# Optimization experiments

Measured on AMD Instinct MI355X. Metric: run time of the kernel, lower is better.

## Reference

```python
import jax, jax.numpy as jnp
import numpy as np

B, N, C_IN, C_OUT, K, D_EMB = 64, 2048, 64, 64, 3, 10

def setup_inputs() -> dict:
    key = jax.random.key(0)
    k1, k2, k3, k4 = jax.random.split(key, 4)
    x = jax.random.normal(k1, (B, N, C_IN), dtype=jnp.float32)
    node_embeddings = jax.random.normal(k2, (N, D_EMB), dtype=jnp.float32)
    weights_pool = jax.random.normal(k3, (D_EMB, K, C_IN, C_OUT), dtype=jnp.float32) * 0.1
    bias_pool = jax.random.normal(k4, (D_EMB, C_OUT), dtype=jnp.float32) * 0.1
    return {"x": x, "node_embeddings": node_embeddings,
            "weights_pool": weights_pool, "bias_pool": bias_pool, "cheb_k": K}

def reference(x, node_embeddings, weights_pool, bias_pool, cheb_k):
    n = node_embeddings.shape[0]
    # adaptive adjacency: softmax over rows of relu(E E^T)
    supports = jax.nn.softmax(jax.nn.relu(node_embeddings @ node_embeddings.T), axis=1)  # [N,N]
    support_set = [jnp.eye(n, dtype=x.dtype), supports]
    for _ in range(2, cheb_k):
        support_set.append(2.0 * supports @ support_set[-1] - support_set[-2])
    supports_k = jnp.stack(support_set, axis=0)                     # [K,N,N]
    # per-node weights/bias generated from embedding
    weights = jnp.einsum('nd,dkio->nkio', node_embeddings, weights_pool)  # [N,K,Ci,Co]
    bias = node_embeddings @ bias_pool                               # [N,Co]
    # graph conv: gather Chebyshev-filtered features then per-node grouped GEMM
    x_g = jnp.einsum('knm,bmc->bnkc', supports_k, x)                 # [B,N,K,Ci]
    out = jnp.einsum('bnki,nkio->bno', x_g, weights) + bias          # [B,N,Co]
    return out
```

## Files before the change

### kernel.cpp

```cpp
#include <hip/hip_runtime.h>

typedef __attribute__((ext_vector_type(8))) short short8;
typedef __attribute__((ext_vector_type(4))) float f32x4;
typedef __attribute__((ext_vector_type(4))) unsigned short us4;
typedef __attribute__((ext_vector_type(8))) unsigned short us8;

constexpr int Bb = 64, Nn = 2048, CI = 64, CO = 64, KK = 3, DE = 10;
constexpr int NW = Bb * CI;
constexpr int WPSZ = KK * CI * CO;

__device__ __forceinline__ unsigned short f2bf(float f) {
  unsigned u = __float_as_uint(f);
  u += 0x7fff + ((u >> 16) & 1);
  return (unsigned short)(u >> 16);
}
__device__ __forceinline__ float bf2f(unsigned short h) {
  return __uint_as_float(((unsigned)h) << 16);
}
__device__ __forceinline__ void gl2lds16(const void* g, void* l) {
  __builtin_amdgcn_global_load_lds(
      (const __attribute__((address_space(1))) void*)g,
      (__attribute__((address_space(3))) void*)l, 16, 0, 0);
}

__global__ __launch_bounds__(256) void supports_kernel(
    const float* __restrict__ E, unsigned short* __restrict__ S) {
  const int n = blockIdx.x, t = threadIdx.x;
  __shared__ float red[256];
  float emb[DE];
#pragma unroll
  for (int d = 0; d < DE; d++) emb[d] = E[n * DE + d];
  float v[8], lmax = -1e30f;
#pragma unroll
  for (int j = 0; j < 8; j++) {
    const int m = t + j * 256;
    float dot = 0.f;
#pragma unroll
    for (int d = 0; d < DE; d++) dot += emb[d] * E[m * DE + d];
    v[j] = fmaxf(dot, 0.f);
    lmax = fmaxf(lmax, v[j]);
  }
  red[t] = lmax;
  __syncthreads();
  for (int s = 128; s > 0; s >>= 1) {
    if (t < s) red[t] = fmaxf(red[t], red[t + s]);
    __syncthreads();
  }
  const float rowmax = red[0];
  __syncthreads();
  float lsum = 0.f;
#pragma unroll
  for (int j = 0; j < 8; j++) { v[j] = __expf(v[j] - rowmax); lsum += v[j]; }
  red[t] = lsum;
  __syncthreads();
  for (int s = 128; s > 0; s >>= 1) {
    if (t < s) red[t] += red[t + s];
    __syncthreads();
  }
  const float inv = 1.f / red[0];
#pragma unroll
  for (int j = 0; j < 8; j++) S[(size_t)n * Nn + t + j * 256] = f2bf(v[j] * inv);
}

__global__ __launch_bounds__(256) void x2xt_kernel(
    const float* __restrict__ x, unsigned short* __restrict__ Xrow,
    unsigned short* __restrict__ XT) {
  __shared__ float T[64 * 65];
  const int b = blockIdx.x, n0 = blockIdx.y * 64, t = threadIdx.x;
  const int i4 = (t & 15) * 4;
#pragma unroll
  for (int j = 0; j < 4; j++) {
    const int r = j * 16 + (t >> 4);
    const float4 v =
        *(const float4*)(x + (size_t)b * (Nn * CI) + (size_t)(n0 + r) * CI + i4);
    us4 o; o.x = f2bf(v.x); o.y = f2bf(v.y); o.z = f2bf(v.z); o.w = f2bf(v.w);
    *(us4*)(Xrow + (size_t)(n0 + r) * NW + b * CI + i4) = o;
    T[r * 65 + i4 + 0] = v.x; T[r * 65 + i4 + 1] = v.y;
    T[r * 65 + i4 + 2] = v.z; T[r * 65 + i4 + 3] = v.w;
  }
  __syncthreads();
  const int i = t >> 2, c0 = (t & 3) * 16;
  us8 p0, p1;
#pragma unroll
  for (int j = 0; j < 8; j++) p0[j] = f2bf(T[(c0 + j) * 65 + i]);
#pragma unroll
  for (int j = 0; j < 8; j++) p1[j] = f2bf(T[(c0 + 8 + j) * 65 + i]);
  unsigned short* dst = XT + (size_t)(b * CI + i) * Nn + n0 + c0;
  *(us8*)(dst) = p0;
  *(us8*)(dst + 8) = p1;
}

__global__ __launch_bounds__(256) void mfma_gemm(
    const unsigned short* __restrict__ A, const unsigned short* __restrict__ Bt,
    const unsigned short* __restrict__ Xsub, unsigned short* __restrict__ Crow,
    unsigned short* __restrict__ Ct, int mode) {
  __shared__ unsigned short sm[16384];
  unsigned short* As = sm;
  unsigned short* Bs = sm + 8192;
  const int t = threadIdx.x, lane = t & 63, wave = t >> 6;
  const int n0 = blockIdx.x * 128, m0 = blockIdx.y * 128;
  const int wm = (wave & 1) * 64, wn = (wave >> 1) * 64;
  const int lr = lane & 15, lq = lane >> 4;

  f32x4 acc[4][4] = {};
  const int srow = lane >> 3;
  const int schunk = (lane & 7) ^ srow;

  for (int k0 = 0; k0 < 2048; k0 += 64) {
    __syncthreads();
#pragma unroll
    for (int j = 0; j < 4; j++) {
      const int r0 = (wave * 4 + j) * 8;
      gl2lds16(A  + (size_t)(m0 + r0 + srow) * 2048 + k0 + schunk * 8, As + r0 * 64);
      gl2lds16(Bt + (size_t)(n0 + r0 + srow) * 2048 + k0 + schunk * 8, Bs + r0 * 64);
    }
    __syncthreads();
#pragma unroll
    for (int ks = 0; ks < 2; ks++) {
      short8 af[4], bfr[4];
#pragma unroll
      for (int i = 0; i < 4; i++) {
        const int m = wm + i * 16 + lr;
        const int slot = (ks * 4 + lq) ^ (m & 7);
        af[i] = *(const short8*)(As + m * 64 + slot * 8);
      }
#pragma unroll
      for (int j = 0; j < 4; j++) {
        const int n = wn + j * 16 + lr;
        const int slot = (ks * 4 + lq) ^ (n & 7);
        bfr[j] = *(const short8*)(Bs + n * 64 + slot * 8);
      }
#pragma unroll
      for (int i = 0; i < 4; i++)
#pragma unroll
        for (int j = 0; j < 4; j++)
          acc[i][j] = __builtin_amdgcn_mfma_f32_16x16x32_bf16(af[i], bfr[j], acc[i][j], 0, 0, 0);
    }
  }

  __syncthreads();
#pragma unroll
  for (int i = 0; i < 4; i++) {
#pragma unroll
    for (int r = 0; r < 4; r++) {
      const int m = wm + i * 16 + lq * 4 + r;
      const int sw = (m & 7) ^ ((m >> 3) & 7);
#pragma unroll
      for (int j = 0; j < 4; j++) {
        const int n = wn + j * 16 + lr;
        sm[m * 128 + (((n >> 3) ^ sw) * 8) + (n & 7)] = f2bf(acc[i][j][r]);
      }
    }
  }
  __syncthreads();

  {
    const int rr = t >> 4, cc = (t & 15) * 8;
#pragma unroll
    for (int p = 0; p < 8; p++) {
      const int m = p * 16 + rr;
      const int slot = (cc >> 3) ^ (m & 7) ^ ((m >> 3) & 7);
      us8 v = *(const us8*)(sm + m * 128 + slot * 8);
      if (mode == 1) {
        const us8 xv = *(const us8*)(Xsub + (size_t)(m0 + m) * NW + n0 + cc);
#pragma unroll
        for (int q = 0; q < 8; q++) v[q] = f2bf(2.f * bf2f(v[q]) - bf2f(xv[q]));
      }
      *(us8*)(Crow + (size_t)(m0 + m) * NW + n0 + cc) = v;
    }
  }
  if (mode == 0) {
    const int w = t >> 4, mc = (t & 15) * 8;
#pragma unroll
    for (int p = 0; p < 8; p++) {
      const int n = p * 16 + w;
      us8 v;
#pragma unroll
      for (int q = 0; q < 8; q++) {
        const int m = mc + q;
        v[q] = sm[m * 128 + (((n >> 3) ^ (m & 7) ^ ((m >> 3) & 7)) * 8) + (n & 7)];
      }
      *(us8*)(Ct + (size_t)(n0 + n) * 2048 + m0 + mc) = v;
    }
  }
}

__global__ __launch_bounds__(256) void out_kernel(
    const unsigned short* __restrict__ Xrow, const unsigned short* __restrict__ XG1,
    const unsigned short* __restrict__ XG2, const float* __restrict__ E,
    const float* __restrict__ Wp, const float* __restrict__ bp,
    float* __restrict__ out) {
  constexpr int WP = 72;
  __shared__ unsigned short Wt[KK * CO * WP];
  __shared__ unsigned short Al[KK * Bb * CI];
  __shared__ float biasl[CO];

  const int n = blockIdx.x, t = threadIdx.x, lane = t & 63, wave = t >> 6;

  const unsigned short* srcs[KK] = {Xrow + (size_t)n * NW, XG1 + (size_t)n * NW,
                                    XG2 + (size_t)n * NW};
  const int srow = lane >> 3;
  const int schunk = (lane & 7) ^ srow;
#pragma unroll
  for (int j = 0; j < 6; j++) {
    const int r0 = (wave * 6 + j) * 8;
    const int c = r0 >> 6, b0 = r0 & 63;
    gl2lds16(srcs[c] + (b0 + srow) * 64 + schunk * 8, Al + r0 * 64);
  }

  float emb[DE];
#pragma unroll
  for (int d = 0; d < DE; d++) emb[d] = E[n * DE + d];

#pragma unroll
  for (int j = 0; j < 12; j++) {
    const int idx4 = j * 1024 + t * 4;
    const int c = j >> 2;
    const int i = (j * 16 + (t >> 4)) & 63;
    const int o = (t & 15) * 4;
    f32x4 w = {0.f, 0.f, 0.f, 0.f};
#pragma unroll
    for (int d = 0; d < DE; d++) {
      const float4 wp = *(const float4*)(Wp + (size_t)d * WPSZ + idx4);
      w[0] += emb[d] * wp.x; w[1] += emb[d] * wp.y;
      w[2] += emb[d] * wp.z; w[3] += emb[d] * wp.w;
    }
#pragma unroll
    for (int q = 0; q < 4; q++)
      Wt[c * (CO * WP) + (o + q) * WP + i] = f2bf(w[q]);
  }
  if (t < CO) {
    float bsum = 0.f;
#pragma unroll
    for (int d = 0; d < DE; d++) bsum += emb[d] * bp[d * CO + t];
    biasl[t] = bsum;
  }
  __syncthreads();

  const int lr = lane & 15, lq = lane >> 4;
  f32x4 acc[4] = {};
#pragma unroll
  for (int kt = 0; kt < 6; kt++) {
    const int c = kt >> 1;
    const int i0 = (kt & 1) * 32;
    const short8 bfrag = *(const short8*)(Wt + c * (CO * WP) +
                                          (wave * 16 + lr) * WP + i0 + lq * 8);
#pragma unroll
    for (int mt = 0; mt < 4; mt++) {
      const int b = mt * 16 + lr;
      const int chunk = (kt & 1) * 4 + lq;
      const int slot = chunk ^ (b & 7);
      const short8 afrag = *(const short8*)(Al + (c * 64 + b) * 64 + slot * 8);
      acc[mt] = __builtin_amdgcn_mfma_f32_16x16x32_bf16(afrag, bfrag, acc[mt], 0, 0, 0);
    }
  }

  const float bias_o = biasl[wave * 16 + lr];
#pragma unroll
  for (int mt = 0; mt < 4; mt++) {
#pragma unroll
    for (int r = 0; r < 4; r++) {
      const int b = mt * 16 + lq * 4 + r;
      out[(size_t)b * (Nn * CO) + (size_t)n * CO + wave * 16 + lr] =
          acc[mt][r] + bias_o;
    }
  }
}

extern "C" void kernel_launch(void* const* d_in, const int* in_sizes, int n_in,
                              void* d_out, int out_size, void* d_ws,
                              size_t ws_size, hipStream_t stream) {
  const float* x  = (const float*)d_in[0];
  const float* E  = (const float*)d_in[1];
  const float* Wp = (const float*)d_in[2];
  const float* bp = (const float*)d_in[3];
  float* out = (float*)d_out;

  unsigned short* S    = (unsigned short*)d_ws;
  unsigned short* XT   = S    + (size_t)Nn * Nn;
  unsigned short* Xrow = XT   + (size_t)NW * Nn;
  unsigned short* XG1T = Xrow + (size_t)Nn * NW;
  unsigned short* XG1r = XG1T + (size_t)NW * Nn;
  unsigned short* XG2r = XG1r + (size_t)Nn * NW;

  supports_kernel<<<Nn, 256, 0, stream>>>(E, S);
  x2xt_kernel<<<dim3(Bb, Nn / 64), 256, 0, stream>>>(x, Xrow, XT);

  dim3 g(NW / 128, Nn / 128);
  mfma_gemm<<<g, 256, 0, stream>>>(S, XT,   nullptr, XG1r, XG1T, 0);
  mfma_gemm<<<g, 256, 0, stream>>>(S, XG1T, Xrow,    XG2r, nullptr, 1);

  out_kernel<<<Nn, 256, 0, stream>>>(Xrow, XG1r, XG2r, E, Wp, bp, out);
}
```

Before: 236.2 us.

## Precompute per-node bf16 weights in separate kernel and stream them into out_kernel

Moves generation of the per-node weights and bias out of out_kernel into a new wgen_kernel. That kernel holds the weight-pool slices in registers and reuses them across 64 nodes, then writes bf16 weights in a swizzled layout that matches out_kernel's LDS pattern. out_kernel now loads those weights with async global-to-LDS copies, so each block no longer re-reads the full 10x12K float weight pool. The cost is an extra kernel launch and a write plus read of 2048x12K bf16 weights (about 50MB), which reuses the supports buffer in the reorganized workspace.

```diff
diff --git a/kernel.cpp b/kernel.cpp
--- a/kernel.cpp
+++ b/kernel.cpp
@@ -185,20 +185,79 @@
   }
 }
 
+__global__ __launch_bounds__(256) void wgen_kernel(
+    const float* __restrict__ E, const float* __restrict__ Wp,
+    const float* __restrict__ bp, unsigned short* __restrict__ W_all,
+    float* __restrict__ bias_all) {
+  constexpr int WSP = 24;
+  const int t = threadIdx.x, n0 = blockIdx.x * 64, c = blockIdx.y;
+  __shared__ float El[64 * DE];
+  __shared__ unsigned short Ws[4][64 * WSP];
+
+  for (int idx = t; idx < 64 * DE; idx += 256) El[idx] = E[n0 * DE + idx];
+  __syncthreads();
+
+  if (c == 0) {
+#pragma unroll
+    for (int j = 0; j < 16; j++) {
+      const int idx = j * 256 + t;
+      const int nl = idx >> 6, o = idx & 63;
+      float bsum = 0.f;
+#pragma unroll
+      for (int d = 0; d < DE; d++) bsum += El[nl * DE + d] * bp[d * CO + o];
+      bias_all[(size_t)(n0 + nl) * CO + o] = bsum;
+    }
+  }
+
+  const int o = t & 63, ig = t >> 6;
+  for (int p = 0; p < 4; p++) {
+    float wp[4][DE];
+#pragma unroll
+    for (int j = 0; j < 4; j++) {
+      const int i = p * 16 + ig * 4 + j;
+#pragma unroll
+      for (int d = 0; d < DE; d++)
+        wp[j][d] = Wp[(size_t)d * WPSZ + c * (CI * CO) + i * CO + o];
+    }
+    for (int g = 0; g < 16; g++) {
+#pragma unroll
+      for (int nl = 0; nl < 4; nl++) {
+        const int nn = g * 4 + nl;
+        us4 w;
+#pragma unroll
+        for (int j = 0; j < 4; j++) {
+          float acc = 0.f;
+#pragma unroll
+          for (int d = 0; d < DE; d++) acc += El[nn * DE + d] * wp[j][d];
+          w[j] = f2bf(acc);
+        }
+        *(us4*)&Ws[nl][o * WSP + ig * 4] = w;
+      }
+      __syncthreads();
+#pragma unroll
+      for (int rd = 0; rd < 2; rd++) {
+        const int idx = rd * 256 + t;
+        const int nl = idx >> 7, o2 = (idx >> 1) & 63, h = idx & 1;
+        const us8 v = *(const us8*)&Ws[nl][o2 * WSP + h * 8];
+        *(us8*)(W_all + (size_t)(n0 + g * 4 + nl) * WPSZ +
+                (c * 64 + o2) * 64 + p * 16 + h * 8) = v;
+      }
+      __syncthreads();
+    }
+  }
+}
+
 __global__ __launch_bounds__(256) void out_kernel(
     const unsigned short* __restrict__ Xrow, const unsigned short* __restrict__ XG1,
-    const unsigned short* __restrict__ XG2, const float* __restrict__ E,
-    const float* __restrict__ Wp, const float* __restrict__ bp,
-    float* __restrict__ out) {
-  constexpr int WP = 72;
-  __shared__ unsigned short Wt[KK * CO * WP];
+    const unsigned short* __restrict__ XG2, const unsigned short* __restrict__ W_all,
+    const float* __restrict__ bias_all, float* __restrict__ out) {
+  __shared__ unsigned short Wt[KK * CO * 64];
   __shared__ unsigned short Al[KK * Bb * CI];
-  __shared__ float biasl[CO];
 
   const int n = blockIdx.x, t = threadIdx.x, lane = t & 63, wave = t >> 6;
-
   const unsigned short* srcs[KK] = {Xrow + (size_t)n * NW, XG1 + (size_t)n * NW,
                                     XG2 + (size_t)n * NW};
+  const unsigned short* wsrc = W_all + (size_t)n * WPSZ;
   const int srow = lane >> 3;
   const int schunk = (lane & 7) ^ srow;
 #pragma unroll
@@ -206,56 +265,30 @@
     const int r0 = (wave * 6 + j) * 8;
     const int c = r0 >> 6, b0 = r0 & 63;
     gl2lds16(srcs[c] + (b0 + srow) * 64 + schunk * 8, Al + r0 * 64);
-  }
-
-  float emb[DE];
-#pragma unroll
-  for (int d = 0; d < DE; d++) emb[d] = E[n * DE + d];
-
-#pragma unroll
-  for (int j = 0; j < 12; j++) {
-    const int idx4 = j * 1024 + t * 4;
-    const int c = j >> 2;
-    const int i = (j * 16 + (t >> 4)) & 63;
-    const int o = (t & 15) * 4;
-    f32x4 w = {0.f, 0.f, 0.f, 0.f};
-#pragma unroll
-    for (int d = 0; d < DE; d++) {
-      const float4 wp = *(const float4*)(Wp + (size_t)d * WPSZ + idx4);
-      w[0] += emb[d] * wp.x; w[1] += emb[d] * wp.y;
-      w[2] += emb[d] * wp.z; w[3] += emb[d] * wp.w;
-    }
-#pragma unroll
-    for (int q = 0; q < 4; q++)
-      Wt[c * (CO * WP) + (o + q) * WP + i] = f2bf(w[q]);
-  }
-  if (t < CO) {
-    float bsum = 0.f;
-#pragma unroll
-    for (int d = 0; d < DE; d++) bsum += emb[d] * bp[d * CO + t];
-    biasl[t] = bsum;
-  }
-  __syncthreads();
+    gl2lds16(wsrc + (r0 + srow) * 64 + schunk * 8, Wt + r0 * 64);
+  }
 
   const int lr = lane & 15, lq = lane >> 4;
+  const float bias_o = bias_all[(size_t)n * CO + wave * 16 + lr];
+  __syncthreads();
+
   f32x4 acc[4] = {};
 #pragma unroll
   for (int kt = 0; kt < 6; kt++) {
     const int c = kt >> 1;
-    const int i0 = (kt & 1) * 32;
-    const short8 bfrag = *(const short8*)(Wt + c * (CO * WP) +
-                                          (wave * 16 + lr) * WP + i0 + lq * 8);
+    const int chunk = (kt & 1) * 4 + lq;
+    const int o = wave * 16 + lr;
+    const short8 bfrag =
+        *(const short8*)(Wt + (c * 64 + o) * 64 + (chunk ^ (o & 7)) * 8);
 #pragma unroll
     for (int mt = 0; mt < 4; mt++) {
       const int b = mt * 16 + lr;
-      const int chunk = (kt & 1) * 4 + lq;
-      const int slot = chunk ^ (b & 7);
-      const short8 afrag = *(const short8*)(Al + (c * 64 + b) * 64 + slot * 8);
+      const short8 afrag =
+          *(const short8*)(Al + (c * 64 + b) * 64 + (chunk ^ (b & 7)) * 8);
       acc[mt] = __builtin_amdgcn_mfma_f32_16x16x32_bf16(afrag, bfrag, acc[mt], 0, 0, 0);
     }
   }
 
-  const float bias_o = biasl[wave * 16 + lr];
 #pragma unroll
   for (int mt = 0; mt < 4; mt++) {
 #pragma unroll
@@ -276,12 +309,15 @@
   const float* bp = (const float*)d_in[3];
   float* out = (float*)d_out;
 
-  unsigned short* S    = (unsigned short*)d_ws;
+  unsigned short* ws   = (unsigned short*)d_ws;
+  unsigned short* Xrow = ws;
+  unsigned short* XG1r = Xrow + (size_t)Nn * NW;
+  unsigned short* XG2r = XG1r + (size_t)Nn * NW;
+  unsigned short* S    = XG2r + (size_t)Nn * NW;
   unsigned short* XT   = S    + (size_t)Nn * Nn;
-  unsigned short* Xrow = XT   + (size_t)NW * Nn;
-  unsigned short* XG1T = Xrow + (size_t)Nn * NW;
-  unsigned short* XG1r = XG1T + (size_t)NW * Nn;
-  unsigned short* XG2r = XG1r + (size_t)Nn * NW;
+  unsigned short* XG1T = XT   + (size_t)NW * Nn;
+  unsigned short* W_all = S;
+  float* bias_all = (float*)(W_all + (size_t)Nn * WPSZ);
 
   supports_kernel<<<Nn, 256, 0, stream>>>(E, S);
   x2xt_kernel<<<dim3(Bb, Nn / 64), 256, 0, stream>>>(x, Xrow, XT);
@@ -290,5 +326,6 @@
   mfma_gemm<<<g, 256, 0, stream>>>(S, XT,   nullptr, XG1r, XG1T, 0);
   mfma_gemm<<<g, 256, 0, stream>>>(S, XG1T, Xrow,    XG2r, nullptr, 1);
 
-  out_kernel<<<Nn, 256, 0, stream>>>(Xrow, XG1r, XG2r, E, Wp, bp, out);
-}
+  wgen_kernel<<<dim3(Nn / 64, KK), 256, 0, stream>>>(E, Wp, bp, W_all, bias_all);
+  out_kernel<<<Nn, 256, 0, stream>>>(Xrow, XG1r, XG2r, W_all, bias_all, out);
+}
```

New measurement: 266.6 us. 1.13x slower.
